# Optimization experiments

Measured on AMD Instinct MI355X. Metric: run time of the kernel, lower is better.

Reference implementation:

```python
import jax, jax.numpy as jnp
import numpy as np

VDE, VEN = 30000, 30000
D, H, M = 620, 1000, 1000
B, S, T = 32, 20, 20  # T = decoder steps = y.shape[1]-1


def _lstm(xe, Wih, Whh, b):
    """Single-layer LSTM, batch_first. xe: [B,L,D] -> [B,L,H]. PyTorch gate order i,f,g,o.
    (b = b_ih + b_hh; mathematically identical to PyTorch's two biases.)"""
    Bn = xe.shape[0]
    Hn = Whh.shape[1]
    xp = jnp.einsum('bld,gd->blg', xe, Wih) + b  # [B,L,4H]

    def step(carry, xt):
        h, c = carry
        gates = xt + h @ Whh.T
        i, f, g, o = jnp.split(gates, 4, axis=-1)
        c = jax.nn.sigmoid(f) * c + jax.nn.sigmoid(i) * jnp.tanh(g)
        h = jax.nn.sigmoid(o) * jnp.tanh(c)
        return (h, c), h

    init = (jnp.zeros((Bn, Hn), xe.dtype), jnp.zeros((Bn, Hn), xe.dtype))
    _, hs = jax.lax.scan(step, init, jnp.swapaxes(xp, 0, 1))
    return jnp.swapaxes(hs, 0, 1)


def setup_inputs() -> dict:
    key = jax.random.key(0)
    ks = jax.random.split(key, 24)

    def w(k, shape, s=0.05):
        return jax.random.normal(k, shape, jnp.float32) * s

    return {
        'x': jax.random.randint(ks[0], (B, S), 0, VDE),
        'y': jax.random.randint(ks[1], (B, T + 1), 0, VEN),
        'emb_de': w(ks[2], (VDE, D)),
        'emb_en': w(ks[3], (VEN, D)),
        'enc_Wih': w(ks[4], (4 * H, D)), 'enc_Whh': w(ks[5], (4 * H, H)), 'enc_b': jnp.zeros((4 * H,), jnp.float32),
        'dec_Wih': w(ks[6], (4 * H, D)), 'dec_Whh': w(ks[7], (4 * H, H)), 'dec_b': jnp.zeros((4 * H,), jnp.float32),
        'Wa_w': w(ks[8], (H, H)), 'Wa_b': jnp.zeros((H,), jnp.float32),
        'Ua_w': w(ks[9], (H, H)), 'Ua_b': jnp.zeros((H,), jnp.float32),
        'Va_w': w(ks[10], (H,)), 'Va_b': jnp.zeros((), jnp.float32),
        'U_w': w(ks[11], (2 * M, H)), 'U_b': jnp.zeros((2 * M,), jnp.float32),
        'V_w': w(ks[12], (2 * M, D)), 'V_b': jnp.zeros((2 * M,), jnp.float32),
        'C_w': w(ks[13], (2 * M, H)), 'C_b': jnp.zeros((2 * M,), jnp.float32),
        'W_w': w(ks[14], (VEN, M)), 'W_b': jnp.zeros((VEN,), jnp.float32),
    }


def reference(x, y, emb_de, emb_en, enc_Wih, enc_Whh, enc_b,
              dec_Wih, dec_Whh, dec_b, Wa_w, Wa_b, Ua_w, Ua_b, Va_w, Va_b,
              U_w, U_b, V_w, V_b, C_w, C_b, W_w, W_b):
    e_de = emb_de[x]                 # [B,S,D]
    e_en = emb_en[y]                 # [B,T+1,D]
    enc_h = _lstm(e_de, enc_Wih, enc_Whh, enc_b)          # [B,S,H]
    dec_h = _lstm(e_en[:, :-1], dec_Wih, dec_Whh, dec_b)  # [B,T,H]

    # Bahdanau additive attention (fused broadcast-add + tanh + Va)
    Wa = jnp.einsum('bth,gh->btg', dec_h, Wa_w) + Wa_b    # [B,T,H]
    Ua = jnp.einsum('bsh,gh->bsg', enc_h, Ua_w) + Ua_b    # [B,S,H]
    scores = jnp.einsum('bsth,h->bst', jnp.tanh(Ua[:, :, None, :] + Wa[:, None, :, :]), Va_w) + Va_b  # [B,S,T]

    attn = jax.nn.softmax(scores, axis=1)                 # softmax over source positions
    context = jnp.einsum('bst,bsh->bth', attn, enc_h)     # [B,T,H]

    # deep-output maxout layer, batched over all t
    u = (jnp.einsum('bth,gh->btg', dec_h, U_w) + U_b
         + jnp.einsum('btd,gd->btg', e_en[:, :-1], V_w) + V_b
         + jnp.einsum('bth,gh->btg', context, C_w) + C_b)  # [B,T,2M]
    t_max = jnp.max(u.reshape(B, T, M, 2), axis=-1)        # [B,T,M]

    logits = jnp.einsum('btm,vm->btv', t_max, W_w) + W_b   # [B,T,Ven]
    logp = jax.nn.log_softmax(logits, axis=-1)
    labels = y[:, 1:]                                      # [B,T]
    nll = -jnp.take_along_axis(logp, labels[:, :, None], axis=-1)[..., 0]  # [B,T]
    # original: sum over t of NLLLoss(mean over batch)
    loss = jnp.sum(jnp.mean(nll, axis=0))
    return loss
```

## Files before the change

### kernel.cpp

```cpp
#include <hip/hip_runtime.h>
#include <math.h>

#define VEN_  30000
#define Dd    620
#define Hh    1000
#define Gg    4000
#define Mm    1000
#define Bb    32
#define Ss    20
#define Tt    20
#define NST   470

typedef __attribute__((ext_vector_type(8))) short short8b;
typedef __attribute__((ext_vector_type(4))) float f32x4;

typedef __attribute__((address_space(1))) void GASV;
typedef __attribute__((address_space(3))) void LASV;
#define GLOAD_LDS16(g, l) \
    __builtin_amdgcn_global_load_lds((GASV*)(const void*)(g), (LASV*)(void*)(l), 16, 0, 0)

__device__ __forceinline__ float sigf(float x) { return 1.0f / (1.0f + __expf(-x)); }
__device__ __forceinline__ ushort f2bf(float f) {
    unsigned u = __float_as_uint(f);
    u = (u + 0x7fffu + ((u >> 16) & 1u)) >> 16;
    return (ushort)u;
}
__device__ __forceinline__ float bf2f(ushort u) { return __uint_as_float(((unsigned)u) << 16); }
__device__ __forceinline__ short8b cvt8(float4 a, float4 b) {
    ushort v[8];
    v[0] = f2bf(a.x); v[1] = f2bf(a.y); v[2] = f2bf(a.z); v[3] = f2bf(a.w);
    v[4] = f2bf(b.x); v[5] = f2bf(b.y); v[6] = f2bf(b.z); v[7] = f2bf(b.w);
    return *(short8b*)v;
}

__global__ void conv_bf16(const float* __restrict__ in, int K,
                          ushort* __restrict__ out, int ostride, int kp8, int total) {
    int idx = blockIdx.x * 256 + threadIdx.x;
    if (idx >= total) return;
    int rr = idx / kp8, c8 = (idx % kp8) * 8;
    const float* src = in + (size_t)rr * K + c8;
    short8b o;
    if (c8 + 7 < K) {
        o = cvt8(*(const float4*)src, *(const float4*)(src + 4));
    } else {
        ushort v[8];
        #pragma unroll
        for (int j = 0; j < 8; ++j) v[j] = (c8 + j < K) ? f2bf(src[j]) : (ushort)0;
        o = *(short8b*)v;
    }
    *(short8b*)&out[(size_t)rr * ostride + c8] = o;
}

struct ConvJob { const float* src; ushort* dst; int K; int ostride; int kp8; unsigned end; };
struct ConvJobs { ConvJob j[9]; };

__global__ void conv_multi(ConvJobs jobs, unsigned total) {
    unsigned v = blockIdx.x * 256 + threadIdx.x;
    if (v >= total) return;
    int ji = 0;
    while (v >= jobs.j[ji].end) ++ji;
    unsigned base = ji ? jobs.j[ji - 1].end : 0;
    unsigned local = v - base;
    const ConvJob J = jobs.j[ji];
    int rr = local / J.kp8, c8 = (local % J.kp8) * 8;
    const float* src = J.src + (size_t)rr * J.K + c8;
    short8b o;
    if (c8 + 7 < J.K) {
        o = cvt8(*(const float4*)src, *(const float4*)(src + 4));
    } else {
        ushort w[8];
        #pragma unroll
        for (int j = 0; j < 8; ++j) w[j] = (c8 + j < J.K) ? f2bf(src[j]) : (ushort)0;
        o = *(short8b*)w;
    }
    *(short8b*)&J.dst[(size_t)rr * J.ostride + c8] = o;
}

__global__ void add3(const float* __restrict__ a, const float* __restrict__ b,
                     const float* __restrict__ c, float* __restrict__ o, int n) {
    int i = blockIdx.x * 256 + threadIdx.x;
    if (i < n) o[i] = a[i] + b[i] + c[i];
}

__global__ void gather_emb_bf16(const float* __restrict__ emb, const int* __restrict__ toks,
                                int tstride, ushort* __restrict__ out, int ostride) {
    int idx = blockIdx.x * 256 + threadIdx.x;
    if (idx >= Bb * Tt * 80) return;
    int row = idx / 80, c8 = (idx % 80) * 8;
    int b = row / Tt, t = row % Tt;
    int tok = toks[b * tstride + t];
    const float* src = emb + (size_t)tok * Dd + c8;
    short8b o;
    if (c8 + 7 < Dd) {
        o = cvt8(*(const float4*)src, *(const float4*)(src + 4));
    } else {
        ushort v[8];
        #pragma unroll
        for (int j = 0; j < 8; ++j) v[j] = (c8 + j < Dd) ? f2bf(src[j]) : (ushort)0;
        o = *(short8b*)v;
    }
    *(short8b*)&out[(size_t)row * ostride + c8] = o;
}

template <int MODE>
__global__ __launch_bounds__(256) void gemm_nt(
    const ushort* __restrict__ A, int lda,
    const ushort* __restrict__ B, int ldb,
    const float* __restrict__ bias,
    float* __restrict__ C, int ldc,
    float* __restrict__ pm, float* __restrict__ ps,
    ushort* __restrict__ Cb,
    int M, int N, int Kp, int MT)
{
    __shared__ __align__(16) ushort As[128 * 64];
    __shared__ __align__(16) ushort Bs[128 * 64];
    const int tid = threadIdx.x;
    const int w = tid >> 6, lane = tid & 63;
    const int wm = w >> 1, wn = w & 1;
    const int lhi = lane >> 4, llo = lane & 15;

    int nblk = gridDim.x;
    int q = nblk >> 3, r = nblk & 7;
    int xcd = blockIdx.x & 7, lo = blockIdx.x >> 3;
    int wg = ((xcd < r) ? xcd * (q + 1) : r * (q + 1) + (xcd - r) * q) + lo;
    int mt = wg % MT, nt = wg / MT;
    const int row0 = mt * 128, col0 = nt * 128;

    const int lr8 = lane >> 3;
    const int cs = (lane & 7) ^ lr8;
    const ushort* pA[4];
    const ushort* pB[4];
    #pragma unroll
    for (int qq = 0; qq < 4; ++qq) {
        int seg = w + qq * 4;
        int ra = row0 + seg * 8 + lr8; if (ra > M - 1) ra = M - 1;
        int rb = col0 + seg * 8 + lr8; if (rb > N - 1) rb = N - 1;
        pA[qq] = A + (size_t)ra * lda + cs * 8;
        pB[qq] = B + (size_t)rb * ldb + cs * 8;
    }

    f32x4 acc[4][4] = {};

    for (int kk = 0; kk < Kp; kk += 64) {
        #pragma unroll
        for (int qq = 0; qq < 4; ++qq) {
            int seg = w + qq * 4;
            GLOAD_LDS16(pA[qq] + kk, (char*)As + (seg << 10));
            GLOAD_LDS16(pB[qq] + kk, (char*)Bs + (seg << 10));
        }
        __syncthreads();
        #pragma unroll
        for (int ks = 0; ks < 2; ++ks) {
            short8b af[4], bg[4];
            #pragma unroll
            for (int i = 0; i < 4; ++i) {
                int Ra = wm * 64 + i * 16 + llo;
                int ca = (ks * 4 + lhi) ^ (Ra & 7);
                af[i] = *(const short8b*)((const char*)As + Ra * 128 + (ca << 4));
                int Rb = wn * 64 + i * 16 + llo;
                int cb = (ks * 4 + lhi) ^ (Rb & 7);
                bg[i] = *(const short8b*)((const char*)Bs + Rb * 128 + (cb << 4));
            }
            #pragma unroll
            for (int i = 0; i < 4; ++i)
                #pragma unroll
                for (int j = 0; j < 4; ++j)
                    acc[i][j] = __builtin_amdgcn_mfma_f32_16x16x32_bf16(af[i], bg[j], acc[i][j], 0, 0, 0);
        }
        __syncthreads();
    }

    if (MODE == 0) {
        #pragma unroll
        for (int i = 0; i < 4; ++i) {
            #pragma unroll
            for (int reg = 0; reg < 4; ++reg) {
                int row = row0 + wm * 64 + i * 16 + lhi * 4 + reg;
                if (row >= M) continue;
                #pragma unroll
                for (int j = 0; j < 4; ++j) {
                    int col = col0 + wn * 64 + j * 16 + llo;
                    if (col < N)
                        C[(size_t)row * ldc + col] = acc[i][j][reg] + (bias ? bias[col] : 0.f);
                }
            }
        }
    } else if (MODE == 1) {
        #pragma unroll
        for (int i = 0; i < 4; ++i) {
            #pragma unroll
            for (int reg = 0; reg < 4; ++reg) {
                int row = row0 + wm * 64 + i * 16 + lhi * 4 + reg;
                float vals[4], vmax = -1e30f;
                #pragma unroll
                for (int j = 0; j < 4; ++j) {
                    int col = col0 + wn * 64 + j * 16 + llo;
                    vals[j] = (col < N) ? (acc[i][j][reg] + bias[col]) : -1e30f;
                    vmax = fmaxf(vmax, vals[j]);
                }
                #pragma unroll
                for (int off = 8; off; off >>= 1) vmax = fmaxf(vmax, __shfl_xor(vmax, off, 16));
                float se = 0.f;
                #pragma unroll
                for (int j = 0; j < 4; ++j) {
                    int col = col0 + wn * 64 + j * 16 + llo;
                    if (col < N) se += __expf(vals[j] - vmax);
                }
                #pragma unroll
                for (int off = 8; off; off >>= 1) se += __shfl_xor(se, off, 16);
                if (llo == 0 && row < M) {
                    pm[(size_t)row * NST + nt * 2 + wn] = vmax;
                    ps[(size_t)row * NST + nt * 2 + wn] = se;
                }
            }
        }
    } else {
        #pragma unroll
        for (int i = 0; i < 4; ++i) {
            #pragma unroll
            for (int reg = 0; reg < 4; ++reg) {
                int row = row0 + wm * 64 + i * 16 + lhi * 4 + reg;
                #pragma unroll
                for (int j = 0; j < 4; ++j) {
                    int col = col0 + wn * 64 + j * 16 + llo;
                    float v = acc[i][j][reg] + bias[col < N ? col : 0];
                    float o = fmaxf(v, __shfl_xor(v, 1));
                    if (((llo & 1) == 0) && row < M && col + 1 < N) {
                        int m = col >> 1;
                        C[(size_t)row * ldc + m] = o;
                        Cb[(size_t)row * 1024 + m] = f2bf(o);
                    }
                }
            }
        }
    }
}

__global__ __launch_bounds__(512) void lstm_step8(
    const float* __restrict__ xpE, const float* __restrict__ xpD,
    const ushort* __restrict__ WE, const ushort* __restrict__ WD,
    float* __restrict__ cE, float* __restrict__ cD,
    ushort* __restrict__ hE, ushort* __restrict__ hD,
    int strideE, int strideD, int t)
{
    __shared__ float gsm[8][32][16];
    const int which = blockIdx.y;
    const float* xp = which ? xpD : xpE;
    const ushort* Whh = which ? WD : WE;
    float* cb = which ? cD : cE;
    ushort* hs = which ? hD : hE;
    const int hstride = which ? strideD : strideE;

    const int tid = threadIdx.x;
    const int wave = tid >> 6, l = tid & 63;
    const int g = wave & 3, half = wave >> 2;
    const int lhi = l >> 4, llo = l & 15;
    const int j0 = blockIdx.x * 16;
    const int jc = (j0 + llo < Hh) ? (j0 + llo) : (Hh - 1);
    const int kbase = half * 512;

    f32x4 acc0 = {0.f, 0.f, 0.f, 0.f};
    f32x4 acc1 = {0.f, 0.f, 0.f, 0.f};

    if (t > 0) {
        const ushort* wp  = Whh + (size_t)(g * Hh + jc) * 1024 + kbase + lhi * 8;
        const ushort* h0p = hs + ((size_t)llo * Tt + (t - 1)) * hstride + kbase + lhi * 8;
        const ushort* h1p = hs + ((size_t)(llo + 16) * Tt + (t - 1)) * hstride + kbase + lhi * 8;
        short8b wreg[4], a0r[4], a1r[4];
        #pragma unroll
        for (int pp = 0; pp < 4; ++pp) {
            wreg[pp] = *(const short8b*)(wp  + pp * 32);
            a0r[pp]  = *(const short8b*)(h0p + pp * 32);
            a1r[pp]  = *(const short8b*)(h1p + pp * 32);
        }
        #pragma unroll
        for (int kk = 0; kk < 16; ++kk) {
            short8b wc = wreg[kk & 3], a0 = a0r[kk & 3], a1 = a1r[kk & 3];
            if (kk + 4 < 16) {
                wreg[kk & 3] = *(const short8b*)(wp  + (kk + 4) * 32);
                a0r[kk & 3]  = *(const short8b*)(h0p + (kk + 4) * 32);
                a1r[kk & 3]  = *(const short8b*)(h1p + (kk + 4) * 32);
            }
            acc0 = __builtin_amdgcn_mfma_f32_16x16x32_bf16(a0, wc, acc0, 0, 0, 0);
            acc1 = __builtin_amdgcn_mfma_f32_16x16x32_bf16(a1, wc, acc1, 0, 0, 0);
        }
    }
    #pragma unroll
    for (int reg = 0; reg < 4; ++reg) {
        gsm[wave][lhi * 4 + reg][llo]      = acc0[reg];
        gsm[wave][16 + lhi * 4 + reg][llo] = acc1[reg];
    }
    __syncthreads();

    {
        int b = tid >> 4, jj = tid & 15;
        int jw = j0 + jj;
        if (jw < Hh) {
            const float* xpr = xp + ((size_t)b * Tt + t) * Gg;
            float vi = gsm[0][b][jj] + gsm[4][b][jj] + xpr[jw];
            float vf = gsm[1][b][jj] + gsm[5][b][jj] + xpr[Hh + jw];
            float vg = gsm[2][b][jj] + gsm[6][b][jj] + xpr[2 * Hh + jw];
            float vo = gsm[3][b][jj] + gsm[7][b][jj] + xpr[3 * Hh + jw];
            float co = cb[(size_t)b * Hh + jw];
            float cn = sigf(vf) * co + sigf(vi) * tanhf(vg);
            float hn = sigf(vo) * tanhf(cn);
            cb[(size_t)b * Hh + jw] = cn;
            hs[((size_t)b * Tt + t) * hstride + jw] = f2bf(hn);
        }
    }
}

__global__ __launch_bounds__(256) void attn_scores(
    const float* __restrict__ Ua, const float* __restrict__ Wa,
    const float* __restrict__ Va_w, const float* __restrict__ Va_b,
    float* __restrict__ scores)
{
    int wave = (blockIdx.x * 256 + threadIdx.x) >> 6;
    int lane = threadIdx.x & 63;
    if (wave >= Bb * Ss * Tt) return;
    int b = wave / (Ss * Tt);
    int rem = wave % (Ss * Tt);
    int s = rem / Tt, t = rem % Tt;
    const float* ua = Ua + (size_t)(b * Ss + s) * Hh;
    const float* wa = Wa + (size_t)(b * Tt + t) * Hh;
    float acc = 0.f;
    for (int h = lane; h < Hh; h += 64)
        acc += tanhf(ua[h] + wa[h]) * Va_w[h];
    #pragma unroll
    for (int off = 32; off; off >>= 1) acc += __shfl_xor(acc, off, 64);
    if (lane == 0) scores[(size_t)(b * Ss + s) * Tt + t] = acc + Va_b[0];
}

__global__ __launch_bounds__(256) void softmax_context(
    const float* __restrict__ scores, const ushort* __restrict__ enc_hb,
    ushort* __restrict__ ctx_out, int ostride)
{
    __shared__ float w[Ss];
    int b = blockIdx.x / Tt, t = blockIdx.x % Tt;
    if (threadIdx.x == 0) {
        float sc[Ss];
        float mx = -1e30f;
        for (int s = 0; s < Ss; ++s) {
            sc[s] = scores[(size_t)(b * Ss + s) * Tt + t];
            mx = fmaxf(mx, sc[s]);
        }
        float sum = 0.f;
        for (int s = 0; s < Ss; ++s) { float e = __expf(sc[s] - mx); w[s] = e; sum += e; }
        float inv = 1.f / sum;
        for (int s = 0; s < Ss; ++s) w[s] *= inv;
    }
    __syncthreads();
    for (int h = threadIdx.x; h < Hh; h += 256) {
        float acc = 0.f;
        #pragma unroll
        for (int s = 0; s < Ss; ++s)
            acc += w[s] * bf2f(enc_hb[((size_t)b * Ss + s) * 1024 + h]);
        ctx_out[(size_t)(b * Tt + t) * ostride + h] = f2bf(acc);
    }
}

__global__ __launch_bounds__(256) void nll_kernel(
    const float* __restrict__ pm, const float* __restrict__ ps,
    const float* __restrict__ tmax, const float* __restrict__ Ww,
    const float* __restrict__ Wb, const int* __restrict__ y,
    float* __restrict__ nll)
{
    __shared__ float sm[4];
    int row = blockIdx.x;
    int tid = threadIdx.x;
    float mx = -1e30f;
    for (int i = tid; i < NST; i += 256) mx = fmaxf(mx, pm[(size_t)row * NST + i]);
    #pragma unroll
    for (int off = 32; off; off >>= 1) mx = fmaxf(mx, __shfl_xor(mx, off, 64));
    if ((tid & 63) == 0) sm[tid >> 6] = mx;
    __syncthreads();
    mx = fmaxf(fmaxf(sm[0], sm[1]), fmaxf(sm[2], sm[3]));
    __syncthreads();
    float s = 0.f;
    for (int i = tid; i < NST; i += 256)
        s += ps[(size_t)row * NST + i] * __expf(pm[(size_t)row * NST + i] - mx);
    #pragma unroll
    for (int off = 32; off; off >>= 1) s += __shfl_xor(s, off, 64);
    if ((tid & 63) == 0) sm[tid >> 6] = s;
    __syncthreads();
    s = sm[0] + sm[1] + sm[2] + sm[3];
    __syncthreads();
    int b = row / Tt, t = row % Tt;
    int lab = y[b * (Tt + 1) + t + 1];
    float d = 0.f;
    for (int m = tid; m < Mm; m += 256)
        d += tmax[(size_t)row * Mm + m] * Ww[(size_t)lab * Mm + m];
    #pragma unroll
    for (int off = 32; off; off >>= 1) d += __shfl_xor(d, off, 64);
    if ((tid & 63) == 0) sm[tid >> 6] = d;
    __syncthreads();
    d = sm[0] + sm[1] + sm[2] + sm[3] + Wb[lab];
    if (tid == 0) nll[row] = (mx + logf(s)) - d;
}

__global__ void loss_kernel(const float* __restrict__ nll, float* __restrict__ out) {
    __shared__ float sm[4];
    float s = 0.f;
    for (int i = threadIdx.x; i < Bb * Tt; i += 256) s += nll[i];
    #pragma unroll
    for (int off = 32; off; off >>= 1) s += __shfl_xor(s, off, 64);
    if ((threadIdx.x & 63) == 0) sm[threadIdx.x >> 6] = s;
    __syncthreads();
    if (threadIdx.x == 0) out[0] = (sm[0] + sm[1] + sm[2] + sm[3]) / (float)Bb;
}

extern "C" void kernel_launch(void* const* d_in, const int* in_sizes, int n_in,
                              void* d_out, int out_size, void* d_ws, size_t ws_size,
                              hipStream_t stream)
{
    const int* x = (const int*)d_in[0];
    const int* y = (const int*)d_in[1];
    const float* emb_de  = (const float*)d_in[2];
    const float* emb_en  = (const float*)d_in[3];
    const float* enc_Wih = (const float*)d_in[4];
    const float* enc_Whh = (const float*)d_in[5];
    const float* enc_b   = (const float*)d_in[6];
    const float* dec_Wih = (const float*)d_in[7];
    const float* dec_Whh = (const float*)d_in[8];
    const float* dec_b   = (const float*)d_in[9];
    const float* Wa_w = (const float*)d_in[10];
    const float* Wa_b = (const float*)d_in[11];
    const float* Ua_w = (const float*)d_in[12];
    const float* Ua_b = (const float*)d_in[13];
    const float* Va_w = (const float*)d_in[14];
    const float* Va_b = (const float*)d_in[15];
    const float* U_w  = (const float*)d_in[16];
    const float* U_b  = (const float*)d_in[17];
    const float* V_w  = (const float*)d_in[18];
    const float* V_b  = (const float*)d_in[19];
    const float* C_w  = (const float*)d_in[20];
    const float* C_b  = (const float*)d_in[21];
    const float* W_w  = (const float*)d_in[22];
    const float* W_b  = (const float*)d_in[23];

    char* base = (char*)d_ws;
    size_t off = 0;
    auto alloc = [&](size_t bytes) { char* p = base + off; off += (bytes + 255) & ~(size_t)255; return p; };

    float*  xp_enc   = (float*)alloc(640ull * 4000 * 4);
    float*  xp_dec   = (float*)alloc(640ull * 4000 * 4);
    float*  Wa       = (float*)alloc(640ull * 1000 * 4);
    float*  Ua       = (float*)alloc(640ull * 1000 * 4);
    float*  scores   = (float*)alloc((size_t)Bb * Ss * Tt * 4);
    float*  pm       = (float*)alloc(640ull * NST * 4);
    float*  ps       = (float*)alloc(640ull * NST * 4);
    float*  nll      = (float*)alloc(640ull * 4);
    float*  c_enc    = (float*)alloc(32ull * 1000 * 4);
    float*  c_dec    = (float*)alloc(32ull * 1000 * 4);
    float*  bias_cat = (float*)alloc(2000ull * 4);
    ushort* e_de_b   = (ushort*)alloc(640ull * 640 * 2);
    ushort* A_cat    = (ushort*)alloc(640ull * 2688 * 2);
    ushort* hs_enc_b = (ushort*)alloc(640ull * 1024 * 2);
    ushort* whh_enc_b= (ushort*)alloc(4000ull * 1024 * 2);
    ushort* whh_dec_b= (ushort*)alloc(4000ull * 1024 * 2);
    ushort* wbig     = (ushort*)alloc(30000ull * 1024 * 2);
    ushort* Wcat_b   = (ushort*)alloc(2000ull * 2688 * 2);
    ushort* Wa_w_b   = (ushort*)alloc(1000ull * 1024 * 2);
    ushort* Ua_w_b   = (ushort*)alloc(1000ull * 1024 * 2);

    ushort* wih_enc_b = wbig;
    ushort* wih_dec_b = wbig + 4000ull * 640;
    ushort* W_w_b     = wbig;

    float*  tmax   = xp_enc + 640ull * 2000;
    ushort* tmax_b = (ushort*)xp_dec;

    dim3 blk(256);

    hipMemsetAsync(c_enc, 0, 2ull * 32 * 1000 * 4, stream);
    hipMemsetAsync(hs_enc_b, 0, 640ull * 1024 * 2, stream);
    hipMemsetAsync(A_cat, 0, 640ull * 2688 * 2, stream);

    ConvJobs jobs;
    unsigned acc = 0;
    auto J = [&](int i, const float* s, ushort* d, int K, int ostr, int kp8, int R) {
        acc += (unsigned)R * kp8;
        jobs.j[i] = ConvJob{s, d, K, ostr, kp8, acc};
    };
    J(0, enc_Whh, whh_enc_b, 1000, 1024, 128, 4000);
    J(1, dec_Whh, whh_dec_b, 1000, 1024, 128, 4000);
    J(2, enc_Wih, wih_enc_b,  620,  640,  80, 4000);
    J(3, dec_Wih, wih_dec_b,  620,  640,  80, 4000);
    J(4, Wa_w,    Wa_w_b,    1000, 1024, 128, 1000);
    J(5, Ua_w,    Ua_w_b,    1000, 1024, 128, 1000);
    J(6, U_w,     Wcat_b,          1000, 2688, 128, 2000);
    J(7, V_w,     Wcat_b + 1024,    620, 2688,  80, 2000);
    J(8, C_w,     Wcat_b + 1664,   1000, 2688, 128, 2000);
    conv_multi<<<dim3((acc + 255) / 256), blk, 0, stream>>>(jobs, acc);
    add3<<<dim3(8), blk, 0, stream>>>(U_b, V_b, C_b, bias_cat, 2000);

    gather_emb_bf16<<<dim3(200), blk, 0, stream>>>(emb_de, x, Ss, e_de_b, 640);
    gather_emb_bf16<<<dim3(200), blk, 0, stream>>>(emb_en, y, Tt + 1, A_cat + 1024, 2688);

    gemm_nt<0><<<dim3(160), blk, 0, stream>>>(e_de_b, 640, wih_enc_b, 640, enc_b,
                                              xp_enc, 4000, nullptr, nullptr, nullptr, 640, 4000, 640, 5);
    gemm_nt<0><<<dim3(160), blk, 0, stream>>>(A_cat + 1024, 2688, wih_dec_b, 640, dec_b,
                                              xp_dec, 4000, nullptr, nullptr, nullptr, 640, 4000, 640, 5);

    conv_bf16<<<dim3(15000), blk, 0, stream>>>(W_w, 1000, W_w_b, 1024, 128, 30000 * 128);

    for (int t = 0; t < Tt; ++t)
        lstm_step8<<<dim3(63, 2), dim3(512), 0, stream>>>(
            xp_enc, xp_dec, whh_enc_b, whh_dec_b, c_enc, c_dec,
            hs_enc_b, A_cat, 1024, 2688, t);

    gemm_nt<0><<<dim3(40), blk, 0, stream>>>(A_cat, 2688, Wa_w_b, 1024, Wa_b,
                                             Wa, 1000, nullptr, nullptr, nullptr, 640, 1000, 1024, 5);
    gemm_nt<0><<<dim3(40), blk, 0, stream>>>(hs_enc_b, 1024, Ua_w_b, 1024, Ua_b,
                                             Ua, 1000, nullptr, nullptr, nullptr, 640, 1000, 1024, 5);

    attn_scores<<<dim3(3200), blk, 0, stream>>>(Ua, Wa, Va_w, Va_b, scores);
    softmax_context<<<dim3(640), blk, 0, stream>>>(scores, hs_enc_b, A_cat + 1664, 2688);

    hipMemsetAsync(tmax_b, 0, 640ull * 1024 * 2, stream);

    gemm_nt<2><<<dim3(80), blk, 0, stream>>>(A_cat, 2688, Wcat_b, 2688, bias_cat,
                                             tmax, 1000, nullptr, nullptr, tmax_b,
                                             640, 2000, 2688, 5);

    gemm_nt<1><<<dim3(1175), blk, 0, stream>>>(tmax_b, 1024, W_w_b, 1024, W_b,
                                               nullptr, 0, pm, ps, nullptr, 640, VEN_, 1024, 5);

    nll_kernel<<<dim3(640), blk, 0, stream>>>(pm, ps, tmax, W_w, W_b, y, nll);
    loss_kernel<<<dim3(1), blk, 0, stream>>>(nll, (float*)d_out);
}
```

Baseline: 604.1 us.

## Persist LSTM with grid barrier, double-buffer GEMM, merge paired launches

```diff
diff --git a/kernel.cpp b/kernel.cpp
--- a/kernel.cpp
+++ b/kernel.cpp
@@ -76,16 +76,15 @@
     *(short8b*)&J.dst[(size_t)rr * J.ostride + c8] = o;
 }
 
-__global__ void add3(const float* __restrict__ a, const float* __restrict__ b,
-                     const float* __restrict__ c, float* __restrict__ o, int n) {
-    int i = blockIdx.x * 256 + threadIdx.x;
-    if (i < n) o[i] = a[i] + b[i] + c[i];
-}
-
-__global__ void gather_emb_bf16(const float* __restrict__ emb, const int* __restrict__ toks,
-                                int tstride, ushort* __restrict__ out, int ostride) {
+__global__ void gather2(const float* __restrict__ embA, const int* __restrict__ tokA,
+                        int strA, ushort* __restrict__ outA, int osA,
+                        const float* __restrict__ embB, const int* __restrict__ tokB,
+                        int strB, ushort* __restrict__ outB, int osB) {
     int idx = blockIdx.x * 256 + threadIdx.x;
     if (idx >= Bb * Tt * 80) return;
+    const float* emb; const int* toks; int tstride; ushort* out; int ostride;
+    if (blockIdx.y == 0) { emb = embA; toks = tokA; tstride = strA; out = outA; ostride = osA; }
+    else                 { emb = embB; toks = tokB; tstride = strB; out = outB; ostride = osB; }
     int row = idx / 80, c8 = (idx % 80) * 8;
     int b = row / Tt, t = row % Tt;
     int tok = toks[b * tstride + t];
@@ -102,18 +101,17 @@
     *(short8b*)&out[(size_t)row * ostride + c8] = o;
 }
 
+struct GemmArgs {
+    const ushort* A; int lda;
+    const ushort* B; int ldb;
+    const float* bias; const float* bias2; const float* bias3;
+    float* C; int ldc;
+    float* pm; float* ps; ushort* Cb;
+    int M, N, Kp, MT;
+};
+
 template <int MODE>
-__global__ __launch_bounds__(256) void gemm_nt(
-    const ushort* __restrict__ A, int lda,
-    const ushort* __restrict__ B, int ldb,
-    const float* __restrict__ bias,
-    float* __restrict__ C, int ldc,
-    float* __restrict__ pm, float* __restrict__ ps,
-    ushort* __restrict__ Cb,
-    int M, int N, int Kp, int MT)
-{
-    __shared__ __align__(16) ushort As[128 * 64];
-    __shared__ __align__(16) ushort Bs[128 * 64];
+__device__ __forceinline__ void gemm_body(ushort* As, ushort* Bs, const GemmArgs g) {
     const int tid = threadIdx.x;
     const int w = tid >> 6, lane = tid & 63;
     const int wm = w >> 1, wn = w & 1;
@@ -123,7 +121,7 @@
     int q = nblk >> 3, r = nblk & 7;
     int xcd = blockIdx.x & 7, lo = blockIdx.x >> 3;
     int wg = ((xcd < r) ? xcd * (q + 1) : r * (q + 1) + (xcd - r) * q) + lo;
-    int mt = wg % MT, nt = wg / MT;
+    int mt = wg % g.MT, nt = wg / g.MT;
     const int row0 = mt * 128, col0 = nt * 128;
 
     const int lr8 = lane >> 3;
@@ -133,22 +131,35 @@
     #pragma unroll
     for (int qq = 0; qq < 4; ++qq) {
         int seg = w + qq * 4;
-        int ra = row0 + seg * 8 + lr8; if (ra > M - 1) ra = M - 1;
-        int rb = col0 + seg * 8 + lr8; if (rb > N - 1) rb = N - 1;
-        pA[qq] = A + (size_t)ra * lda + cs * 8;
-        pB[qq] = B + (size_t)rb * ldb + cs * 8;
+        int ra = row0 + seg * 8 + lr8; if (ra > g.M - 1) ra = g.M - 1;
+        int rb = col0 + seg * 8 + lr8; if (rb > g.N - 1) rb = g.N - 1;
+        pA[qq] = g.A + (size_t)ra * g.lda + cs * 8;
+        pB[qq] = g.B + (size_t)rb * g.ldb + cs * 8;
     }
 
     f32x4 acc[4][4] = {};
 
-    for (int kk = 0; kk < Kp; kk += 64) {
-        #pragma unroll
-        for (int qq = 0; qq < 4; ++qq) {
-            int seg = w + qq * 4;
-            GLOAD_LDS16(pA[qq] + kk, (char*)As + (seg << 10));
-            GLOAD_LDS16(pB[qq] + kk, (char*)Bs + (seg << 10));
-        }
-        __syncthreads();
+    #pragma unroll
+    for (int qq = 0; qq < 4; ++qq) {
+        int seg = w + qq * 4;
+        GLOAD_LDS16(pA[qq], (char*)As + (seg << 10));
+        GLOAD_LDS16(pB[qq], (char*)Bs + (seg << 10));
+    }
+    __syncthreads();
+
+    int cur = 0;
+    for (int kk = 0; kk < g.Kp; kk += 64) {
+        if (kk + 64 < g.Kp) {
+            int nb = (cur ^ 1) << 14;
+            #pragma unroll
+            for (int qq = 0; qq < 4; ++qq) {
+                int seg = w + qq * 4;
+                GLOAD_LDS16(pA[qq] + kk + 64, (char*)As + nb + (seg << 10));
+                GLOAD_LDS16(pB[qq] + kk + 64, (char*)Bs + nb + (seg << 10));
+            }
+        }
+        const char* curA = (const char*)As + (cur << 14);
+        const char* curB = (const char*)Bs + (cur << 14);
         #pragma unroll
         for (int ks = 0; ks < 2; ++ks) {
             short8b af[4], bg[4];
@@ -156,10 +167,10 @@
             for (int i = 0; i < 4; ++i) {
                 int Ra = wm * 64 + i * 16 + llo;
                 int ca = (ks * 4 + lhi) ^ (Ra & 7);
-                af[i] = *(const short8b*)((const char*)As + Ra * 128 + (ca << 4));
+                af[i] = *(const short8b*)(curA + Ra * 128 + (ca << 4));
                 int Rb = wn * 64 + i * 16 + llo;
-                int cb = (ks * 4 + lhi) ^ (Rb & 7);
-                bg[i] = *(const short8b*)((const char*)Bs + Rb * 128 + (cb << 4));
+                int cbs = (ks * 4 + lhi) ^ (Rb & 7);
+                bg[i] = *(const short8b*)(curB + Rb * 128 + (cbs << 4));
             }
             #pragma unroll
             for (int i = 0; i < 4; ++i)
@@ -168,6 +179,7 @@
                     acc[i][j] = __builtin_amdgcn_mfma_f32_16x16x32_bf16(af[i], bg[j], acc[i][j], 0, 0, 0);
         }
         __syncthreads();
+        cur ^= 1;
     }
 
     if (MODE == 0) {
@@ -176,12 +188,12 @@
             #pragma unroll
             for (int reg = 0; reg < 4; ++reg) {
                 int row = row0 + wm * 64 + i * 16 + lhi * 4 + reg;
-                if (row >= M) continue;
+                if (row >= g.M) continue;
                 #pragma unroll
                 for (int j = 0; j < 4; ++j) {
                     int col = col0 + wn * 64 + j * 16 + llo;
-                    if (col < N)
-                        C[(size_t)row * ldc + col] = acc[i][j][reg] + (bias ? bias[col] : 0.f);
+                    if (col < g.N)
+                        g.C[(size_t)row * g.ldc + col] = acc[i][j][reg] + (g.bias ? g.bias[col] : 0.f);
                 }
             }
         }
@@ -195,7 +207,7 @@
                 #pragma unroll
                 for (int j = 0; j < 4; ++j) {
                     int col = col0 + wn * 64 + j * 16 + llo;
-                    vals[j] = (col < N) ? (acc[i][j][reg] + bias[col]) : -1e30f;
+                    vals[j] = (col < g.N) ? (acc[i][j][reg] + g.bias[col]) : -1e30f;
                     vmax = fmaxf(vmax, vals[j]);
                 }
                 #pragma unroll
@@ -204,13 +216,13 @@
                 #pragma unroll
                 for (int j = 0; j < 4; ++j) {
                     int col = col0 + wn * 64 + j * 16 + llo;
-                    if (col < N) se += __expf(vals[j] - vmax);
+                    if (col < g.N) se += __expf(vals[j] - vmax);
                 }
                 #pragma unroll
                 for (int off = 8; off; off >>= 1) se += __shfl_xor(se, off, 16);
-                if (llo == 0 && row < M) {
-                    pm[(size_t)row * NST + nt * 2 + wn] = vmax;
-                    ps[(size_t)row * NST + nt * 2 + wn] = se;
+                if (llo == 0 && row < g.M) {
+                    g.pm[(size_t)row * NST + nt * 2 + wn] = vmax;
+                    g.ps[(size_t)row * NST + nt * 2 + wn] = se;
                 }
             }
         }
@@ -223,12 +235,14 @@
                 #pragma unroll
                 for (int j = 0; j < 4; ++j) {
                     int col = col0 + wn * 64 + j * 16 + llo;
-                    float v = acc[i][j][reg] + bias[col < N ? col : 0];
+                    int cc = col < g.N ? col : 0;
+                    float bv = g.bias[cc] + (g.bias2 ? g.bias2[cc] : 0.f) + (g.bias3 ? g.bias3[cc] : 0.f);
+                    float v = acc[i][j][reg] + bv;
                     float o = fmaxf(v, __shfl_xor(v, 1));
-                    if (((llo & 1) == 0) && row < M && col + 1 < N) {
+                    if (((llo & 1) == 0) && row < g.M && col + 1 < g.N) {
                         int m = col >> 1;
-                        C[(size_t)row * ldc + m] = o;
-                        Cb[(size_t)row * 1024 + m] = f2bf(o);
+                        g.C[(size_t)row * g.ldc + m] = o;
+                        g.Cb[(size_t)row * 1024 + m] = f2bf(o);
                     }
                 }
             }
@@ -236,18 +250,30 @@
     }
 }
 
-__global__ __launch_bounds__(512) void lstm_step8(
+template <int MODE>
+__global__ __launch_bounds__(256) void gemm_one(GemmArgs g) {
+    __shared__ __align__(16) ushort As[2 * 128 * 64];
+    __shared__ __align__(16) ushort Bs[2 * 128 * 64];
+    gemm_body<MODE>(As, Bs, g);
+}
+
+__global__ __launch_bounds__(256) void gemm_pair(GemmArgs g0, GemmArgs g1) {
+    __shared__ __align__(16) ushort As[2 * 128 * 64];
+    __shared__ __align__(16) ushort Bs[2 * 128 * 64];
+    if (blockIdx.y == 0) gemm_body<0>(As, Bs, g0);
+    else                 gemm_body<0>(As, Bs, g1);
+}
+
+__global__ __launch_bounds__(512) void lstm_all(
     const float* __restrict__ xpE, const float* __restrict__ xpD,
     const ushort* __restrict__ WE, const ushort* __restrict__ WD,
-    float* __restrict__ cE, float* __restrict__ cD,
     ushort* __restrict__ hE, ushort* __restrict__ hD,
-    int strideE, int strideD, int t)
+    int strideE, int strideD, unsigned* __restrict__ bar)
 {
     __shared__ float gsm[8][32][16];
     const int which = blockIdx.y;
     const float* xp = which ? xpD : xpE;
     const ushort* Whh = which ? WD : WE;
-    float* cb = which ? cD : cE;
     ushort* hs = which ? hD : hE;
     const int hstride = which ? strideD : strideE;
 
@@ -258,54 +284,65 @@
     const int j0 = blockIdx.x * 16;
     const int jc = (j0 + llo < Hh) ? (j0 + llo) : (Hh - 1);
     const int kbase = half * 512;
-
-    f32x4 acc0 = {0.f, 0.f, 0.f, 0.f};
-    f32x4 acc1 = {0.f, 0.f, 0.f, 0.f};
-
-    if (t > 0) {
-        const ushort* wp  = Whh + (size_t)(g * Hh + jc) * 1024 + kbase + lhi * 8;
-        const ushort* h0p = hs + ((size_t)llo * Tt + (t - 1)) * hstride + kbase + lhi * 8;
-        const ushort* h1p = hs + ((size_t)(llo + 16) * Tt + (t - 1)) * hstride + kbase + lhi * 8;
-        short8b wreg[4], a0r[4], a1r[4];
-        #pragma unroll
-        for (int pp = 0; pp < 4; ++pp) {
-            wreg[pp] = *(const short8b*)(wp  + pp * 32);
-            a0r[pp]  = *(const short8b*)(h0p + pp * 32);
-            a1r[pp]  = *(const short8b*)(h1p + pp * 32);
-        }
-        #pragma unroll
-        for (int kk = 0; kk < 16; ++kk) {
-            short8b wc = wreg[kk & 3], a0 = a0r[kk & 3], a1 = a1r[kk & 3];
-            if (kk + 4 < 16) {
-                wreg[kk & 3] = *(const short8b*)(wp  + (kk + 4) * 32);
-                a0r[kk & 3]  = *(const short8b*)(h0p + (kk + 4) * 32);
-                a1r[kk & 3]  = *(const short8b*)(h1p + (kk + 4) * 32);
-            }
-            acc0 = __builtin_amdgcn_mfma_f32_16x16x32_bf16(a0, wc, acc0, 0, 0, 0);
-            acc1 = __builtin_amdgcn_mfma_f32_16x16x32_bf16(a1, wc, acc1, 0, 0, 0);
-        }
-    }
-    #pragma unroll
-    for (int reg = 0; reg < 4; ++reg) {
-        gsm[wave][lhi * 4 + reg][llo]      = acc0[reg];
-        gsm[wave][16 + lhi * 4 + reg][llo] = acc1[reg];
-    }
-    __syncthreads();
-
-    {
-        int b = tid >> 4, jj = tid & 15;
-        int jw = j0 + jj;
-        if (jw < Hh) {
-            const float* xpr = xp + ((size_t)b * Tt + t) * Gg;
-            float vi = gsm[0][b][jj] + gsm[4][b][jj] + xpr[jw];
-            float vf = gsm[1][b][jj] + gsm[5][b][jj] + xpr[Hh + jw];
-            float vg = gsm[2][b][jj] + gsm[6][b][jj] + xpr[2 * Hh + jw];
-            float vo = gsm[3][b][jj] + gsm[7][b][jj] + xpr[3 * Hh + jw];
-            float co = cb[(size_t)b * Hh + jw];
-            float cn = sigf(vf) * co + sigf(vi) * tanhf(vg);
-            float hn = sigf(vo) * tanhf(cn);
-            cb[(size_t)b * Hh + jw] = cn;
-            hs[((size_t)b * Tt + t) * hstride + jw] = f2bf(hn);
+    const ushort* wp = Whh + (size_t)(g * Hh + jc) * 1024 + kbase + lhi * 8;
+
+    const int ub = tid >> 4, ujj = tid & 15;
+    const int ujw = j0 + ujj;
+    const float* xpr = xp + (size_t)ub * Tt * Gg;
+    float creg = 0.f;
+
+    for (int t = 0; t < Tt; ++t) {
+        f32x4 acc0 = {0.f, 0.f, 0.f, 0.f};
+        f32x4 acc1 = {0.f, 0.f, 0.f, 0.f};
+        if (t > 0) {
+            const ushort* h0p = hs + ((size_t)llo * Tt + (t - 1)) * hstride + kbase + lhi * 8;
+            const ushort* h1p = hs + ((size_t)(llo + 16) * Tt + (t - 1)) * hstride + kbase + lhi * 8;
+            short8b wreg[4], a0r[4], a1r[4];
+            #pragma unroll
+            for (int pp = 0; pp < 4; ++pp) {
+                wreg[pp] = *(const short8b*)(wp  + pp * 32);
+                a0r[pp]  = *(const short8b*)(h0p + pp * 32);
+                a1r[pp]  = *(const short8b*)(h1p + pp * 32);
+            }
+            #pragma unroll
+            for (int kk = 0; kk < 16; ++kk) {
+                short8b wc = wreg[kk & 3], a0 = a0r[kk & 3], a1 = a1r[kk & 3];
+                if (kk + 4 < 16) {
+                    wreg[kk & 3] = *(const short8b*)(wp  + (kk + 4) * 32);
+                    a0r[kk & 3]  = *(const short8b*)(h0p + (kk + 4) * 32);
+                    a1r[kk & 3]  = *(const short8b*)(h1p + (kk + 4) * 32);
+                }
+                acc0 = __builtin_amdgcn_mfma_f32_16x16x32_bf16(a0, wc, acc0, 0, 0, 0);
+                acc1 = __builtin_amdgcn_mfma_f32_16x16x32_bf16(a1, wc, acc1, 0, 0, 0);
+            }
+        }
+        #pragma unroll
+        for (int reg = 0; reg < 4; ++reg) {
+            gsm[wave][lhi * 4 + reg][llo]      = acc0[reg];
+            gsm[wave][16 + lhi * 4 + reg][llo] = acc1[reg];
+        }
+        __syncthreads();
+        if (ujw < Hh) {
+            const float* xq = xpr + (size_t)t * Gg;
+            float vi = gsm[0][ub][ujj] + gsm[4][ub][ujj] + xq[ujw];
+            float vf = gsm[1][ub][ujj] + gsm[5][ub][ujj] + xq[Hh + ujw];
+            float vg = gsm[2][ub][ujj] + gsm[6][ub][ujj] + xq[2 * Hh + ujw];
+            float vo = gsm[3][ub][ujj] + gsm[7][ub][ujj] + xq[3 * Hh + ujw];
+            creg = sigf(vf) * creg + sigf(vi) * tanhf(vg);
+            float hn = sigf(vo) * tanhf(creg);
+            hs[((size_t)ub * Tt + t) * hstride + ujw] = f2bf(hn);
+        }
+        if (t + 1 < Tt) {
+            __syncthreads();
+            if (tid == 0) {
+                __threadfence();
+                atomicAdd(bar, 1u);
+                unsigned target = 126u * (unsigned)(t + 1);
+                while (__hip_atomic_load(bar, __ATOMIC_RELAXED, __HIP_MEMORY_SCOPE_AGENT) < target)
+                    __builtin_amdgcn_s_sleep(2);
+                __threadfence();
+            }
+            __syncthreads();
         }
     }
 }
@@ -450,12 +487,10 @@
     float*  pm       = (float*)alloc(640ull * NST * 4);
     float*  ps       = (float*)alloc(640ull * NST * 4);
     float*  nll      = (float*)alloc(640ull * 4);
-    float*  c_enc    = (float*)alloc(32ull * 1000 * 4);
-    float*  c_dec    = (float*)alloc(32ull * 1000 * 4);
-    float*  bias_cat = (float*)alloc(2000ull * 4);
     ushort* e_de_b   = (ushort*)alloc(640ull * 640 * 2);
     ushort* A_cat    = (ushort*)alloc(640ull * 2688 * 2);
     ushort* hs_enc_b = (ushort*)alloc(640ull * 1024 * 2);
+    unsigned* bar    = (unsigned*)alloc(256);
     ushort* whh_enc_b= (ushort*)alloc(4000ull * 1024 * 2);
     ushort* whh_dec_b= (ushort*)alloc(4000ull * 1024 * 2);
     ushort* wbig     = (ushort*)alloc(30000ull * 1024 * 2);
@@ -472,9 +507,7 @@
 
     dim3 blk(256);
 
-    hipMemsetAsync(c_enc, 0, 2ull * 32 * 1000 * 4, stream);
-    hipMemsetAsync(hs_enc_b, 0, 640ull * 1024 * 2, stream);
-    hipMemsetAsync(A_cat, 0, 640ull * 2688 * 2, stream);
+    hipMemsetAsync(A_cat, 0, 640ull * 2688 * 2 + 640ull * 1024 * 2 + 256, stream);
 
     ConvJobs jobs;
     unsigned acc = 0;
@@ -492,39 +525,39 @@
     J(7, V_w,     Wcat_b + 1024,    620, 2688,  80, 2000);
     J(8, C_w,     Wcat_b + 1664,   1000, 2688, 128, 2000);
     conv_multi<<<dim3((acc + 255) / 256), blk, 0, stream>>>(jobs, acc);
-    add3<<<dim3(8), blk, 0, stream>>>(U_b, V_b, C_b, bias_cat, 2000);
-
-    gather_emb_bf16<<<dim3(200), blk, 0, stream>>>(emb_de, x, Ss, e_de_b, 640);
-    gather_emb_bf16<<<dim3(200), blk, 0, stream>>>(emb_en, y, Tt + 1, A_cat + 1024, 2688);
-
-    gemm_nt<0><<<dim3(160), blk, 0, stream>>>(e_de_b, 640, wih_enc_b, 640, enc_b,
-                                              xp_enc, 4000, nullptr, nullptr, nullptr, 640, 4000, 640, 5);
-    gemm_nt<0><<<dim3(160), blk, 0, stream>>>(A_cat + 1024, 2688, wih_dec_b, 640, dec_b,
-                                              xp_dec, 4000, nullptr, nullptr, nullptr, 640, 4000, 640, 5);
+
+    gather2<<<dim3(200, 2), blk, 0, stream>>>(emb_de, x, Ss, e_de_b, 640,
+                                              emb_en, y, Tt + 1, A_cat + 1024, 2688);
+
+    GemmArgs ge = {e_de_b, 640, wih_enc_b, 640, enc_b, nullptr, nullptr,
+                   xp_enc, 4000, nullptr, nullptr, nullptr, 640, 4000, 640, 5};
+    GemmArgs gd = {A_cat + 1024, 2688, wih_dec_b, 640, dec_b, nullptr, nullptr,
+                   xp_dec, 4000, nullptr, nullptr, nullptr, 640, 4000, 640, 5};
+    gemm_pair<<<dim3(160, 2), blk, 0, stream>>>(ge, gd);
 
     conv_bf16<<<dim3(15000), blk, 0, stream>>>(W_w, 1000, W_w_b, 1024, 128, 30000 * 128);
 
-    for (int t = 0; t < Tt; ++t)
-        lstm_step8<<<dim3(63, 2), dim3(512), 0, stream>>>(
-            xp_enc, xp_dec, whh_enc_b, whh_dec_b, c_enc, c_dec,
-            hs_enc_b, A_cat, 1024, 2688, t);
-
-    gemm_nt<0><<<dim3(40), blk, 0, stream>>>(A_cat, 2688, Wa_w_b, 1024, Wa_b,
-                                             Wa, 1000, nullptr, nullptr, nullptr, 640, 1000, 1024, 5);
-    gemm_nt<0><<<dim3(40), blk, 0, stream>>>(hs_enc_b, 1024, Ua_w_b, 1024, Ua_b,
-                                             Ua, 1000, nullptr, nullptr, nullptr, 640, 1000, 1024, 5);
+    lstm_all<<<dim3(63, 2), dim3(512), 0, stream>>>(
+        xp_enc, xp_dec, whh_enc_b, whh_dec_b, hs_enc_b, A_cat, 1024, 2688, bar);
+
+    GemmArgs gw = {A_cat, 2688, Wa_w_b, 1024, Wa_b, nullptr, nullptr,
+                   Wa, 1000, nullptr, nullptr, nullptr, 640, 1000, 1024, 5};
+    GemmArgs gu = {hs_enc_b, 1024, Ua_w_b, 1024, Ua_b, nullptr, nullptr,
+                   Ua, 1000, nullptr, nullptr, nullptr, 640, 1000, 1024, 5};
+    gemm_pair<<<dim3(40, 2), blk, 0, stream>>>(gw, gu);
 
     attn_scores<<<dim3(3200), blk, 0, stream>>>(Ua, Wa, Va_w, Va_b, scores);
     softmax_context<<<dim3(640), blk, 0, stream>>>(scores, hs_enc_b, A_cat + 1664, 2688);
 
     hipMemsetAsync(tmax_b, 0, 640ull * 1024 * 2, stream);
 
-    gemm_nt<2><<<dim3(80), blk, 0, stream>>>(A_cat, 2688, Wcat_b, 2688, bias_cat,
-                                             tmax, 1000, nullptr, nullptr, tmax_b,
-                                             640, 2000, 2688, 5);
-
-    gemm_nt<1><<<dim3(1175), blk, 0, stream>>>(tmax_b, 1024, W_w_b, 1024, W_b,
-                                               nullptr, 0, pm, ps, nullptr, 640, VEN_, 1024, 5);
+    GemmArgs gm = {A_cat, 2688, Wcat_b, 2688, U_b, V_b, C_b,
+                   tmax, 1000, nullptr, nullptr, tmax_b, 640, 2000, 2688, 5};
+    gemm_one<2><<<dim3(80), blk, 0, stream>>>(gm);
+
+    GemmArgs gl = {tmax_b, 1024, W_w_b, 1024, W_b, nullptr, nullptr,
+                   nullptr, 0, pm, ps, nullptr, 640, VEN_, 1024, 5};
+    gemm_one<1><<<dim3(1175), blk, 0, stream>>>(gl);
 
     nll_kernel<<<dim3(640), blk, 0, stream>>>(pm, ps, tmax, W_w, W_b, y, nll);
     loss_kernel<<<dim3(1), blk, 0, stream>>>(nll, (float*)d_out);
```

Result: slower. 694.7 us (+15.0%).
